# Performance work log

Hardware: AMD Instinct MI355X
Metric: run time of the kernel (lower is better)

## Reference

```python
import jax, jax.numpy as jnp
import numpy as np

B, S, DIM = 4, 1024, 2048
NH, NKV, HD = 16, 4, 128
G = NH // NKV  # query heads per kv head


def _rope(t, cos, sin):
    # t: (B, S, H, HD); cos/sin: (S, HD//2). Llama-style pairwise rotation.
    tr = t.reshape(*t.shape[:-1], HD // 2, 2)
    t_r, t_i = tr[..., 0], tr[..., 1]
    c = cos[None, :, None, :]
    s = sin[None, :, None, :]
    out_r = t_r * c - t_i * s
    out_i = t_r * s + t_i * c
    return jnp.stack([out_r, out_i], axis=-1).reshape(t.shape)


def setup_inputs() -> dict:
    key = jax.random.key(0)
    ks = jax.random.split(key, 5)
    x = jax.random.normal(ks[0], (B, S, DIM), dtype=jnp.float32)
    # Standard RoPE frequencies
    inv_freq = 1.0 / (10000.0 ** (jnp.arange(0, HD, 2, dtype=jnp.float32) / HD))
    ang = jnp.outer(jnp.arange(S, dtype=jnp.float32), inv_freq)  # (S, HD//2)
    freqs_cos = jnp.cos(ang)
    freqs_sin = jnp.sin(ang)
    # Additive causal mask (1,1,S,S)
    causal = jnp.tril(jnp.ones((S, S), dtype=bool))
    attention_mask = jnp.where(causal, 0.0, -1e9).astype(jnp.float32)[None, None]
    sc = 0.02
    wq = jax.random.normal(ks[1], (NH * HD, DIM), dtype=jnp.float32) * sc
    wk = jax.random.normal(ks[2], (NKV * HD, DIM), dtype=jnp.float32) * sc
    wv = jax.random.normal(ks[3], (NKV * HD, DIM), dtype=jnp.float32) * sc
    wo = jax.random.normal(ks[4], (DIM, NH * HD), dtype=jnp.float32) * sc
    return {"x": x, "freqs_cos": freqs_cos, "freqs_sin": freqs_sin,
            "attention_mask": attention_mask, "wq": wq, "wk": wk, "wv": wv, "wo": wo}


def reference(x, freqs_cos, freqs_sin, attention_mask, wq, wk, wv, wo):
    b, s, _ = x.shape
    q = (x @ wq.T).reshape(b, s, NH, HD)
    k = (x @ wk.T).reshape(b, s, NKV, HD)
    v = (x @ wv.T).reshape(b, s, NKV, HD)
    q = _rope(q, freqs_cos, freqs_sin)
    k = _rope(k, freqs_cos, freqs_sin)
    # kv cache (pre-repeat, as in the torch module)
    new_kv_cache = (k, v)
    # GQA attention: broadcast KV heads across query-head groups instead of
    # materializing repeat_kv (identical math).
    qh = q.transpose(0, 2, 1, 3).reshape(b, NKV, G, s, HD)  # (b, kv, g, s, d)
    kh = k.transpose(0, 2, 1, 3)                             # (b, kv, s, d)
    vh = v.transpose(0, 2, 1, 3)
    scale = 1.0 / jnp.sqrt(jnp.asarray(HD, dtype=x.dtype))
    scores = jnp.einsum('bkgqd,bksd->bkgqs', qh, kh) * scale
    scores = scores + attention_mask[:, :, None]  # (1,1,1,S,S) broadcast
    attn = jax.nn.softmax(scores, axis=-1)
    out = jnp.einsum('bkgqs,bksd->bkgqd', attn, vh)
    out = out.reshape(b, NH, s, HD).transpose(0, 2, 1, 3).reshape(b, s, NH * HD)
    out = out @ wo.T
    return (out, new_kv_cache)
```

## Files before the change

### kernel.cpp

```cpp
#include <hip/hip_runtime.h>

typedef __bf16 bf16;
typedef __bf16 bf16x8 __attribute__((ext_vector_type(8)));
typedef __bf16 bf16x4 __attribute__((ext_vector_type(4)));
typedef float  f32x4  __attribute__((ext_vector_type(4)));

#define AS1 __attribute__((address_space(1)))
#define AS3 __attribute__((address_space(3)))

__device__ __forceinline__ void gload16(void* g, void* l) {
  __builtin_amdgcn_global_load_lds((AS1 void*)g, (AS3 void*)l, 16, 0, 0);
}

__global__ void cast_all(const float4* __restrict__ x,  const float4* __restrict__ wq,
                         const float4* __restrict__ wk, const float4* __restrict__ wv,
                         const float4* __restrict__ wo,
                         bf16x4* __restrict__ xb, bf16x4* __restrict__ wqb,
                         bf16x4* __restrict__ wkvb, bf16x4* __restrict__ wob) {
  long i = (long)blockIdx.x * 256 + threadIdx.x;
  float4 v; bf16x4* dp;
  if (i < 2097152)      { v = x[i];            dp = xb + i; }
  else if (i < 3145728) { v = wq[i - 2097152]; dp = wqb + (i - 2097152); }
  else if (i < 3407872) { v = wk[i - 3145728]; dp = wkvb + (i - 3145728); }
  else if (i < 3670016) { v = wv[i - 3407872]; dp = wkvb + 262144 + (i - 3407872); }
  else                  { v = wo[i - 3670016]; dp = wob + (i - 3670016); }
  bf16x4 o;
  o[0] = (bf16)v.x; o[1] = (bf16)v.y; o[2] = (bf16)v.z; o[3] = (bf16)v.w;
  *dp = o;
}

#define PH_OPEN12 \
  asm volatile("s_waitcnt lgkmcnt(8)" ::: "memory"); \
  __builtin_amdgcn_s_barrier(); \
  asm volatile("s_waitcnt lgkmcnt(0)" ::: "memory"); \
  __builtin_amdgcn_sched_barrier(0); \
  __builtin_amdgcn_s_setprio(1);

#define PH_OPEN \
  __builtin_amdgcn_s_barrier(); \
  asm volatile("s_waitcnt lgkmcnt(0)" ::: "memory"); \
  __builtin_amdgcn_sched_barrier(0); \
  __builtin_amdgcn_s_setprio(1);

#define PH_CLOSE \
  __builtin_amdgcn_s_setprio(0); \
  __builtin_amdgcn_sched_barrier(0); \
  __builtin_amdgcn_s_barrier();

#define MFMAQ(q) \
  _Pragma("unroll") for (int kk = 0; kk < 2; kk++) \
  _Pragma("unroll") for (int m2 = 0; m2 < 2; m2++) \
  _Pragma("unroll") for (int ni = 0; ni < NFR; ni++) \
    acc[(q)*2+m2][ni] = __builtin_amdgcn_mfma_f32_16x16x32_bf16(af[m2][kk], bfr[ni][kk], acc[(q)*2+m2][ni], 0, 0, 0);

template<int NFR>
__global__ __launch_bounds__(512, 2) void gemm8(const bf16* __restrict__ A,
                                                const bf16* __restrict__ Bt,
                                                int N, int epi,
                                                float* __restrict__ Cf,
                                                bf16* __restrict__ qbb,
                                                bf16* __restrict__ kbf,
                                                float* __restrict__ kcache,
                                                float* __restrict__ vcache,
                                                bf16* __restrict__ vtb,
                                                const float* __restrict__ fc,
                                                const float* __restrict__ fs) {
  __shared__ __align__(16) char As[2][32768];
  __shared__ __align__(16) char Bs[2][8192 * NFR];
  const int t = threadIdx.x;
  const int w = t >> 6, l = t & 63, lr = l & 15, lh = l >> 4;
  const int wr = w >> 2, wc = w & 3;
  const int m0 = blockIdx.y << 8, n0 = blockIdx.x * (NFR * 64);

  f32x4 acc[8][NFR];
#pragma unroll
  for (int i = 0; i < 8; i++)
#pragma unroll
    for (int j = 0; j < NFR; j++) acc[i][j] = {0.f, 0.f, 0.f, 0.f};

  auto stA = [&](int buf, int half, int kt) {
#pragma unroll
    for (int p = 0; p < 2; p++) {
      int c = t + (p << 9);
      int rl = c >> 3, sl = c & 7, gs = sl ^ (rl & 7);
      gload16((void*)(A + (long)(m0 + (half << 7) + rl) * 2048 + (kt << 6) + (gs << 3)),
              &As[buf][(half << 14) + (c << 4)]);
    }
  };
  auto stB = [&](int buf, int half, int kt) {
#pragma unroll
    for (int p = 0; p < NFR / 2; p++) {
      int c = t + (p << 9);
      int rl = c >> 3, sl = c & 7, gs = sl ^ (rl & 7);
      gload16((void*)(Bt + (long)(n0 + half * (NFR * 32) + rl) * 2048 + (kt << 6) + (gs << 3)),
              &Bs[buf][half * (NFR * 4096) + (c << 4)]);
    }
  };
  auto rdA = [&](int buf, int mi, int kk) -> bf16x8 {
    int row = (wr << 7) + (mi << 4) + lr;
    int sl  = ((kk << 2) | lh) ^ (row & 7);
    return *(const bf16x8*)(&As[buf][row * 128 + (sl << 4)]);
  };
  auto rdB = [&](int buf, int ni, int kk) -> bf16x8 {
    int row = wc * (NFR * 16) + (ni << 4) + lr;
    int sl  = ((kk << 2) | lh) ^ (row & 7);
    return *(const bf16x8*)(&Bs[buf][row * 128 + (sl << 4)]);
  };

  stB(0, 0, 0); stB(0, 1, 0);
  stA(0, 0, 0); stA(0, 1, 0);
  stB(1, 0, 1); stB(1, 1, 1);
  if constexpr (NFR == 4) { asm volatile("s_waitcnt vmcnt(4)" ::: "memory"); }
  else                    { asm volatile("s_waitcnt vmcnt(2)" ::: "memory"); }
  __builtin_amdgcn_s_barrier();

  const int NI = 16;
  for (int j = 0; j < NI; j++) {
    const int ktE = 2 * j, ktO = 2 * j + 1;
    const bool last = (j == NI - 1);
    bf16x8 bfr[NFR][2], af[2][2];

#pragma unroll
    for (int ni = 0; ni < NFR; ni++) { bfr[ni][0] = rdB(0, ni, 0); bfr[ni][1] = rdB(0, ni, 1); }
    af[0][0] = rdA(0, 0, 0); af[0][1] = rdA(0, 0, 1);
    af[1][0] = rdA(0, 1, 0); af[1][1] = rdA(0, 1, 1);
    stA(1, 0, ktO);
    PH_OPEN12; MFMAQ(0); PH_CLOSE;

    af[0][0] = rdA(0, 2, 0); af[0][1] = rdA(0, 2, 1);
    af[1][0] = rdA(0, 3, 0); af[1][1] = rdA(0, 3, 1);
    stA(1, 1, ktO);
    PH_OPEN; MFMAQ(1); PH_CLOSE;

    af[0][0] = rdA(0, 4, 0); af[0][1] = rdA(0, 4, 1);
    af[1][0] = rdA(0, 5, 0); af[1][1] = rdA(0, 5, 1);
    if (!last) stB(0, 0, ktE + 2);
    PH_OPEN; MFMAQ(2); PH_CLOSE;

    af[0][0] = rdA(0, 6, 0); af[0][1] = rdA(0, 6, 1);
    af[1][0] = rdA(0, 7, 0); af[1][1] = rdA(0, 7, 1);
    if (!last) stB(0, 1, ktE + 2);
    PH_OPEN;  MFMAQ(3);
    __builtin_amdgcn_s_setprio(0);
    __builtin_amdgcn_sched_barrier(0);
    if (last)               { asm volatile("s_waitcnt vmcnt(0)" ::: "memory"); }
    else if constexpr (NFR == 4) { asm volatile("s_waitcnt vmcnt(4)" ::: "memory"); }
    else                    { asm volatile("s_waitcnt vmcnt(2)" ::: "memory"); }
    __builtin_amdgcn_s_barrier();

#pragma unroll
    for (int ni = 0; ni < NFR; ni++) { bfr[ni][0] = rdB(1, ni, 0); bfr[ni][1] = rdB(1, ni, 1); }
    af[0][0] = rdA(1, 0, 0); af[0][1] = rdA(1, 0, 1);
    af[1][0] = rdA(1, 1, 0); af[1][1] = rdA(1, 1, 1);
    if (!last) stA(0, 0, ktE + 2);
    PH_OPEN12; MFMAQ(0); PH_CLOSE;

    af[0][0] = rdA(1, 2, 0); af[0][1] = rdA(1, 2, 1);
    af[1][0] = rdA(1, 3, 0); af[1][1] = rdA(1, 3, 1);
    if (!last) stA(0, 1, ktE + 2);
    PH_OPEN; MFMAQ(1); PH_CLOSE;

    af[0][0] = rdA(1, 4, 0); af[0][1] = rdA(1, 4, 1);
    af[1][0] = rdA(1, 5, 0); af[1][1] = rdA(1, 5, 1);
    if (!last) stB(1, 0, ktO + 2);
    PH_OPEN; MFMAQ(2); PH_CLOSE;

    af[0][0] = rdA(1, 6, 0); af[0][1] = rdA(1, 6, 1);
    af[1][0] = rdA(1, 7, 0); af[1][1] = rdA(1, 7, 1);
    if (!last) stB(1, 1, ktO + 2);
    PH_OPEN; MFMAQ(3);
    __builtin_amdgcn_s_setprio(0);
    __builtin_amdgcn_sched_barrier(0);
    if (!last) {
      if constexpr (NFR == 4) { asm volatile("s_waitcnt vmcnt(4)" ::: "memory"); }
      else                    { asm volatile("s_waitcnt vmcnt(2)" ::: "memory"); }
    }
    __builtin_amdgcn_s_barrier();
  }

  if (epi == 0) {
#pragma unroll
    for (int mi = 0; mi < 8; mi++)
#pragma unroll
      for (int ni = 0; ni < NFR; ni++) {
        int col  = n0 + wc * (NFR * 16) + (ni << 4) + lr;
        int rowb = m0 + (wr << 7) + (mi << 4) + (lh << 2);
#pragma unroll
        for (int r = 0; r < 4; r++)
          Cf[(long)(rowb + r) * N + col] = acc[mi][ni][r];
      }
  } else if (n0 < 2048) {
    const float qs = 0.08838834764831845f;
    const int im = lr & 1;
#pragma unroll
    for (int mi = 0; mi < 8; mi++)
#pragma unroll
      for (int ni = 0; ni < NFR; ni++) {
        int col  = n0 + wc * (NFR * 16) + (ni << 4) + lr;
        int i2   = (col & 127) >> 1;
        int rowb = m0 + (wr << 7) + (mi << 4) + (lh << 2);
#pragma unroll
        for (int r = 0; r < 4; r++) {
          int row = rowb + r, s = row & 1023;
          float c = fc[(s << 6) + i2], sn = fs[(s << 6) + i2];
          float own = acc[mi][ni][r], oth = __shfl_xor(own, 1);
          float xr = im ? oth : own, xi = im ? own : oth;
          float val = im ? (xr * sn + xi * c) : (xr * c - xi * sn);
          qbb[(long)row * 2048 + col] = (bf16)(val * qs);
        }
      }
  } else if (n0 < 2560) {
    const int im = lr & 1;
#pragma unroll
    for (int mi = 0; mi < 8; mi++)
#pragma unroll
      for (int ni = 0; ni < NFR; ni++) {
        int col  = n0 + wc * (NFR * 16) + (ni << 4) + lr;
        int ck   = col - 2048;
        int i2   = (ck & 127) >> 1;
        int rowb = m0 + (wr << 7) + (mi << 4) + (lh << 2);
#pragma unroll
        for (int r = 0; r < 4; r++) {
          int row = rowb + r, s = row & 1023;
          float c = fc[(s << 6) + i2], sn = fs[(s << 6) + i2];
          float own = acc[mi][ni][r], oth = __shfl_xor(own, 1);
          float xr = im ? oth : own, xi = im ? own : oth;
          float val = im ? (xr * sn + xi * c) : (xr * c - xi * sn);
          kbf[(long)row * 512 + ck] = (bf16)val;
          kcache[(long)row * 512 + ck] = val;
        }
      }
  } else {
#pragma unroll
    for (int mi = 0; mi < 8; mi++)
#pragma unroll
      for (int ni = 0; ni < NFR; ni++) {
        int col  = n0 + wc * (NFR * 16) + (ni << 4) + lr;
        int cv   = col - 2560;
        int rowb = m0 + (wr << 7) + (mi << 4) + (lh << 2);
        bf16x4 pk;
#pragma unroll
        for (int r = 0; r < 4; r++) {
          float v = acc[mi][ni][r];
          vcache[(long)(rowb + r) * 512 + cv] = v;
          pk[r] = (bf16)v;
        }
        int b = rowb >> 10, s0 = rowb & 1023;
        *(bf16x4*)(vtb + ((long)((b << 2) + (cv >> 7)) * 128 + (cv & 127)) * 1024 + s0) = pk;
      }
  }
}

__global__ __launch_bounds__(256) void attn_k(const bf16* __restrict__ qb,
                                              const bf16* __restrict__ kb,
                                              const bf16* __restrict__ vt,
                                              bf16* __restrict__ aob) {
  const int bh = blockIdx.x;
  const int qt = 15 - blockIdx.y;
  const int b = bh >> 4, h = bh & 15, kv = h >> 2;
  const int t = threadIdx.x, w = t >> 6, l = t & 63, lr = l & 15, lh = l >> 4;
  __shared__ __align__(16) char Ks[2][16384];
  __shared__ __align__(16) char Vs[2][16384];
  __shared__ __align__(16) bf16 Ps[4][16][72];

  bf16x8 qfrag[4];
  {
    const int qrow = (qt << 6) + (w << 4) + lr;
    const bf16* qp = qb + ((long)(b * 1024 + qrow) << 11) + (h << 7);
#pragma unroll
    for (int kc = 0; kc < 4; kc++) qfrag[kc] = *(const bf16x8*)(qp + (kc << 5) + (lh << 3));
  }

  f32x4 acc[8];
#pragma unroll
  for (int i = 0; i < 8; i++) acc[i] = {0.f, 0.f, 0.f, 0.f};
  float m[4]  = {-1e30f, -1e30f, -1e30f, -1e30f};
  float ls[4] = {0.f, 0.f, 0.f, 0.f};

  const bf16* kg = kb + ((long)b << 19) + (kv << 7);
  const bf16* vg = vt + ((long)(b * 4 + kv) << 17);
  const int nt = qt + 1;

  auto stage = [&](int buf, int tt2) {
    const int kv0 = tt2 << 6;
#pragma unroll
    for (int pass = 0; pass < 4; pass++) {
      int c = t + (pass << 8);
      { int row = c >> 4, slot = c & 15, gs = slot ^ (row & 7);
        gload16((void*)(kg + (long)(kv0 + row) * 512 + (gs << 3)), &Ks[buf][c * 16]); }
      { int row = c >> 3, slot = c & 7,  gs = slot ^ (row & 7);
        gload16((void*)(vg + (long)row * 1024 + kv0 + (gs << 3)), &Vs[buf][c * 16]); }
    }
  };

  stage(0, 0);
  int cur = 0;

  for (int tt = 0; tt < nt; tt++) {
    __syncthreads();
    if (tt + 1 < nt) stage(cur ^ 1, tt + 1);

    f32x4 s4[4];
#pragma unroll
    for (int nf = 0; nf < 4; nf++) s4[nf] = {0.f, 0.f, 0.f, 0.f};
    __builtin_amdgcn_s_setprio(1);
#pragma unroll
    for (int nf = 0; nf < 4; nf++) {
      int key = (nf << 4) + lr;
#pragma unroll
      for (int kc = 0; kc < 4; kc++) {
        bf16x8 kf8 = *(const bf16x8*)(&Ks[cur][0] + key * 256 + (((kc << 6) + (lh << 4)) ^ ((key & 7) << 4)));
        s4[nf] = __builtin_amdgcn_mfma_f32_16x16x32_bf16(qfrag[kc], kf8, s4[nf], 0, 0, 0);
      }
    }
    __builtin_amdgcn_s_setprio(0);

    if (tt == qt) {
      const int kv0 = tt << 6;
#pragma unroll
      for (int nf = 0; nf < 4; nf++) {
        int key = kv0 + (nf << 4) + lr;
#pragma unroll
        for (int r = 0; r < 4; r++) {
          int qg = (qt << 6) + (w << 4) + (lh << 2) + r;
          if (key > qg) s4[nf][r] = -1e30f;
        }
      }
    }

    float mc[4];
#pragma unroll
    for (int r = 0; r < 4; r++)
      mc[r] = fmaxf(fmaxf(s4[0][r], s4[1][r]), fmaxf(s4[2][r], s4[3][r]));
#pragma unroll
    for (int d = 1; d < 16; d <<= 1)
#pragma unroll
      for (int r = 0; r < 4; r++) mc[r] = fmaxf(mc[r], __shfl_xor(mc[r], d));

    int grow = 0;
#pragma unroll
    for (int r = 0; r < 4; r++) grow |= (mc[r] > m[r] + 8.f) ? 1 : 0;
    if (__any(grow)) {
      f32x4 av;
#pragma unroll
      for (int r = 0; r < 4; r++) {
        float mn = fmaxf(m[r], mc[r]);
        float al = __expf(m[r] - mn);
        m[r] = mn; ls[r] *= al; av[r] = al;
      }
#pragma unroll
      for (int hf = 0; hf < 8; hf++) acc[hf] *= av;
    }

    float rs[4] = {0.f, 0.f, 0.f, 0.f};
#pragma unroll
    for (int nf = 0; nf < 4; nf++)
#pragma unroll
      for (int r = 0; r < 4; r++) {
        float p = __expf(s4[nf][r] - m[r]);
        s4[nf][r] = p;
        rs[r] += p;
      }
#pragma unroll
    for (int d = 1; d < 16; d <<= 1)
#pragma unroll
      for (int r = 0; r < 4; r++) rs[r] += __shfl_xor(rs[r], d);
#pragma unroll
    for (int r = 0; r < 4; r++) ls[r] += rs[r];

#pragma unroll
    for (int nf = 0; nf < 4; nf++)
#pragma unroll
      for (int r = 0; r < 4; r++)
        Ps[w][(lh << 2) + r][(nf << 4) + lr] = (bf16)s4[nf][r];

    __builtin_amdgcn_s_setprio(1);
#pragma unroll
    for (int kc = 0; kc < 2; kc++) {
      bf16x8 pf8 = *(const bf16x8*)((const char*)&Ps[w][lr][0] + (kc << 6) + (lh << 4));
#pragma unroll
      for (int hf = 0; hf < 8; hf++) {
        int hd = (hf << 4) + lr;
        bf16x8 vf8 = *(const bf16x8*)(&Vs[cur][0] + hd * 128 + (((kc << 6) + (lh << 4)) ^ ((hd & 7) << 4)));
        acc[hf] = __builtin_amdgcn_mfma_f32_16x16x32_bf16(pf8, vf8, acc[hf], 0, 0, 0);
      }
    }
    __builtin_amdgcn_s_setprio(0);
    cur ^= 1;
  }

  float inv[4];
#pragma unroll
  for (int r = 0; r < 4; r++) inv[r] = 1.f / ls[r];
#pragma unroll
  for (int hf = 0; hf < 8; hf++)
#pragma unroll
    for (int r = 0; r < 4; r++) {
      int qrow = (qt << 6) + (w << 4) + (lh << 2) + r;
      aob[((long)(b * 1024 + qrow) << 11) + (h << 7) + (hf << 4) + lr] = (bf16)(acc[hf][r] * inv[r]);
    }
}

extern "C" void kernel_launch(void* const* d_in, const int* in_sizes, int n_in,
                              void* d_out, int out_size, void* d_ws, size_t ws_size,
                              hipStream_t stream) {
  (void)in_sizes; (void)n_in; (void)out_size; (void)ws_size;
  const float* x  = (const float*)d_in[0];
  const float* fc = (const float*)d_in[1];
  const float* fs = (const float*)d_in[2];
  const float* wq = (const float*)d_in[4];
  const float* wk = (const float*)d_in[5];
  const float* wv = (const float*)d_in[6];
  const float* wo = (const float*)d_in[7];

  float* out    = (float*)d_out;
  float* kcache = out + 8388608;
  float* vcache = out + 10485760;

  char* ws = (char*)d_ws;
  bf16* xb    = (bf16*)(ws);
  bf16* wqkv  = (bf16*)(ws + 16777216);
  bf16* wob   = (bf16*)(ws + 29360128);
  bf16* qbb   = (bf16*)(ws + 54525952);
  bf16* kbf   = (bf16*)(ws + 71303168);
  bf16* vtb   = (bf16*)(ws + 75497472);
  bf16* aob   = (bf16*)(ws + 79691776);

  cast_all<<<18432, 256, 0, stream>>>((const float4*)x, (const float4*)wq,
                                      (const float4*)wk, (const float4*)wv,
                                      (const float4*)wo,
                                      (bf16x4*)xb, (bf16x4*)wqkv,
                                      (bf16x4*)(wqkv + 4194304), (bf16x4*)wob);

  gemm8<4><<<dim3(12, 16), 512, 0, stream>>>(xb, wqkv, 3072, 1, nullptr,
                                             qbb, kbf, kcache, vcache, vtb, fc, fs);

  attn_k<<<dim3(64, 16), 256, 0, stream>>>(qbb, kbf, vtb, aob);

  gemm8<2><<<dim3(16, 16), 512, 0, stream>>>(aob, wob, 2048, 0, out,
                                             nullptr, nullptr, nullptr, nullptr, nullptr,
                                             nullptr, nullptr);
}
```

Before: 174.8 us.

## Preload all A fragments per k-tile and deepen the global-to-LDS prefetch

The GEMM main loop now reads all eight A fragments from LDS at the start of each k-tile instead of reloading two per phase. The global_load_lds issue order is rotated so more tile stages stay in flight, with vmcnt waits relaxed to 6/5 outstanding loads. The aim is to separate LDS reads from the MFMA phases and keep more global loads overlapped with compute. In exchange, register pressure rises (af grows from 4 to 16 bf16x8 vectors) under the 512-thread, 2-block launch bound, which risks spills or lower occupancy.

```diff
diff --git a/kernel.cpp b/kernel.cpp
--- a/kernel.cpp
+++ b/kernel.cpp
@@ -29,13 +29,6 @@
   *dp = o;
 }
 
-#define PH_OPEN12 \
-  asm volatile("s_waitcnt lgkmcnt(8)" ::: "memory"); \
-  __builtin_amdgcn_s_barrier(); \
-  asm volatile("s_waitcnt lgkmcnt(0)" ::: "memory"); \
-  __builtin_amdgcn_sched_barrier(0); \
-  __builtin_amdgcn_s_setprio(1);
-
 #define PH_OPEN \
   __builtin_amdgcn_s_barrier(); \
   asm volatile("s_waitcnt lgkmcnt(0)" ::: "memory"); \
@@ -47,11 +40,14 @@
   __builtin_amdgcn_sched_barrier(0); \
   __builtin_amdgcn_s_barrier();
 
+#define WVM() { if constexpr (NFR == 4) { asm volatile("s_waitcnt vmcnt(6)" ::: "memory"); } \
+                else                    { asm volatile("s_waitcnt vmcnt(5)" ::: "memory"); } }
+
 #define MFMAQ(q) \
   _Pragma("unroll") for (int kk = 0; kk < 2; kk++) \
   _Pragma("unroll") for (int m2 = 0; m2 < 2; m2++) \
   _Pragma("unroll") for (int ni = 0; ni < NFR; ni++) \
-    acc[(q)*2+m2][ni] = __builtin_amdgcn_mfma_f32_16x16x32_bf16(af[m2][kk], bfr[ni][kk], acc[(q)*2+m2][ni], 0, 0, 0);
+    acc[(q)*2+m2][ni] = __builtin_amdgcn_mfma_f32_16x16x32_bf16(af[(q)*2+m2][kk], bfr[ni][kk], acc[(q)*2+m2][ni], 0, 0, 0);
 
 template<int NFR>
 __global__ __launch_bounds__(512, 2) void gemm8(const bf16* __restrict__ A,
@@ -107,74 +103,56 @@
     return *(const bf16x8*)(&Bs[buf][row * 128 + (sl << 4)]);
   };
 
-  stB(0, 0, 0); stB(0, 1, 0);
-  stA(0, 0, 0); stA(0, 1, 0);
-  stB(1, 0, 1); stB(1, 1, 1);
-  if constexpr (NFR == 4) { asm volatile("s_waitcnt vmcnt(4)" ::: "memory"); }
-  else                    { asm volatile("s_waitcnt vmcnt(2)" ::: "memory"); }
+  stA(0, 0, 0); stA(0, 1, 0); stB(0, 0, 0); stB(0, 1, 0);
+  stA(1, 0, 1); stA(1, 1, 1); stB(1, 0, 1);
+  WVM();
   __builtin_amdgcn_s_barrier();
 
   const int NI = 16;
   for (int j = 0; j < NI; j++) {
-    const int ktE = 2 * j, ktO = 2 * j + 1;
     const bool last = (j == NI - 1);
-    bf16x8 bfr[NFR][2], af[2][2];
+    const int kO = 2 * j + 1;
+    bf16x8 af[8][2], bfr[NFR][2];
 
 #pragma unroll
     for (int ni = 0; ni < NFR; ni++) { bfr[ni][0] = rdB(0, ni, 0); bfr[ni][1] = rdB(0, ni, 1); }
-    af[0][0] = rdA(0, 0, 0); af[0][1] = rdA(0, 0, 1);
-    af[1][0] = rdA(0, 1, 0); af[1][1] = rdA(0, 1, 1);
-    stA(1, 0, ktO);
-    PH_OPEN12; MFMAQ(0); PH_CLOSE;
-
-    af[0][0] = rdA(0, 2, 0); af[0][1] = rdA(0, 2, 1);
-    af[1][0] = rdA(0, 3, 0); af[1][1] = rdA(0, 3, 1);
-    stA(1, 1, ktO);
+#pragma unroll
+    for (int mi = 0; mi < 8; mi++) { af[mi][0] = rdA(0, mi, 0); af[mi][1] = rdA(0, mi, 1); }
+    stB(1, 1, kO);
+    PH_OPEN; MFMAQ(0); PH_CLOSE;
+
+    if (!last) stA(0, 0, kO + 1);
     PH_OPEN; MFMAQ(1); PH_CLOSE;
 
-    af[0][0] = rdA(0, 4, 0); af[0][1] = rdA(0, 4, 1);
-    af[1][0] = rdA(0, 5, 0); af[1][1] = rdA(0, 5, 1);
-    if (!last) stB(0, 0, ktE + 2);
+    if (!last) stA(0, 1, kO + 1);
     PH_OPEN; MFMAQ(2); PH_CLOSE;
 
-    af[0][0] = rdA(0, 6, 0); af[0][1] = rdA(0, 6, 1);
-    af[1][0] = rdA(0, 7, 0); af[1][1] = rdA(0, 7, 1);
-    if (!last) stB(0, 1, ktE + 2);
-    PH_OPEN;  MFMAQ(3);
-    __builtin_amdgcn_s_setprio(0);
-    __builtin_amdgcn_sched_barrier(0);
-    if (last)               { asm volatile("s_waitcnt vmcnt(0)" ::: "memory"); }
-    else if constexpr (NFR == 4) { asm volatile("s_waitcnt vmcnt(4)" ::: "memory"); }
-    else                    { asm volatile("s_waitcnt vmcnt(2)" ::: "memory"); }
-    __builtin_amdgcn_s_barrier();
-
-#pragma unroll
-    for (int ni = 0; ni < NFR; ni++) { bfr[ni][0] = rdB(1, ni, 0); bfr[ni][1] = rdB(1, ni, 1); }
-    af[0][0] = rdA(1, 0, 0); af[0][1] = rdA(1, 0, 1);
-    af[1][0] = rdA(1, 1, 0); af[1][1] = rdA(1, 1, 1);
-    if (!last) stA(0, 0, ktE + 2);
-    PH_OPEN12; MFMAQ(0); PH_CLOSE;
-
-    af[0][0] = rdA(1, 2, 0); af[0][1] = rdA(1, 2, 1);
-    af[1][0] = rdA(1, 3, 0); af[1][1] = rdA(1, 3, 1);
-    if (!last) stA(0, 1, ktE + 2);
-    PH_OPEN; MFMAQ(1); PH_CLOSE;
-
-    af[0][0] = rdA(1, 4, 0); af[0][1] = rdA(1, 4, 1);
-    af[1][0] = rdA(1, 5, 0); af[1][1] = rdA(1, 5, 1);
-    if (!last) stB(1, 0, ktO + 2);
-    PH_OPEN; MFMAQ(2); PH_CLOSE;
-
-    af[0][0] = rdA(1, 6, 0); af[0][1] = rdA(1, 6, 1);
-    af[1][0] = rdA(1, 7, 0); af[1][1] = rdA(1, 7, 1);
-    if (!last) stB(1, 1, ktO + 2);
+    if (!last) stB(0, 0, kO + 1);
     PH_OPEN; MFMAQ(3);
     __builtin_amdgcn_s_setprio(0);
     __builtin_amdgcn_sched_barrier(0);
-    if (!last) {
-      if constexpr (NFR == 4) { asm volatile("s_waitcnt vmcnt(4)" ::: "memory"); }
-      else                    { asm volatile("s_waitcnt vmcnt(2)" ::: "memory"); }
-    }
+    if (last) { asm volatile("s_waitcnt vmcnt(0)" ::: "memory"); }
+    else      { WVM(); }
+    __builtin_amdgcn_s_barrier();
+
+#pragma unroll
+    for (int ni = 0; ni < NFR; ni++) { bfr[ni][0] = rdB(1, ni, 0); bfr[ni][1] = rdB(1, ni, 1); }
+#pragma unroll
+    for (int mi = 0; mi < 8; mi++) { af[mi][0] = rdA(1, mi, 0); af[mi][1] = rdA(1, mi, 1); }
+    if (!last) stB(0, 1, kO + 1);
+    PH_OPEN; MFMAQ(0); PH_CLOSE;
+
+    if (!last) stA(1, 0, kO + 2);
+    PH_OPEN; MFMAQ(1); PH_CLOSE;
+
+    if (!last) stA(1, 1, kO + 2);
+    PH_OPEN; MFMAQ(2); PH_CLOSE;
+
+    if (!last) stB(1, 0, kO + 2);
+    PH_OPEN; MFMAQ(3);
+    __builtin_amdgcn_s_setprio(0);
+    __builtin_amdgcn_sched_barrier(0);
+    if (!last) { WVM(); }
     __builtin_amdgcn_s_barrier();
   }
 
```

Result: slower. 187.0 us (+7.0%).
